# Performance work log

Hardware: AMD Instinct MI355X
Metric: run time of the kernel (lower is better)

The kernel has to match this reference:

```python
import jax, jax.numpy as jnp
import numpy as np

K = 1024
T = 16384
P = 2          # number of lags
N_STAGES = 2   # len(s_list)
EDGE_P = 0.005 # edge density -> avg degree ~5


def setup_inputs() -> dict:
    key = jax.random.key(0)
    kX, kA, ka, kb0, kb1 = jax.random.split(key, 5)
    X = jax.random.normal(kX, (K, T), dtype=jnp.float32)
    # sparse symmetric 0/1 adjacency, zero diagonal
    U = jax.random.uniform(kA, (K, K))
    Ab = (U < EDGE_P)
    Ab = (Ab | Ab.T) & ~jnp.eye(K, dtype=bool)
    A = Ab.astype(jnp.float32)
    alpha = jax.random.normal(ka, (P,), dtype=jnp.float32)
    beta0 = jax.random.normal(kb0, (P,), dtype=jnp.float32)
    beta1 = jax.random.normal(kb1, (P,), dtype=jnp.float32)
    return {"X": X, "A": A, "alpha": alpha, "beta0": beta0, "beta1": beta1}


def _stage_avg_matrices(A):
    """M[r] averages over nodes at shortest-path distance exactly r+1 (rows with
    no stage-r neighbors are all-zero, matching the `if neighbors:` guard)."""
    Ab = A > 0.5
    Af = Ab.astype(jnp.float32)
    reach_prev = jnp.eye(A.shape[0], dtype=bool)  # distance <= 0
    Ms = []
    for _ in range(N_STAGES):
        reach = reach_prev | ((reach_prev.astype(jnp.float32) @ Af) > 0.5)
        exact = reach & ~reach_prev                     # distance == r+1
        exact_f = exact.astype(jnp.float32)
        deg = exact_f.sum(axis=1, keepdims=True)        # (K, 1)
        M = exact_f / jnp.maximum(deg, 1.0)             # zero rows stay zero
        Ms.append(M)
        reach_prev = reach
    return Ms


def reference(X, A, alpha, beta0, beta1):
    K_, T_ = X.shape
    betas = [beta0, beta1]
    Ms = _stage_avg_matrices(A)
    # one dense aggregation per stage over ALL time steps, then slice lags
    MXs = [M @ X for M in Ms]                           # each (K, T)
    Y = jnp.zeros((K_, T_ - P), dtype=X.dtype)
    for lag in range(1, P + 1):
        sl = slice(P - lag, T_ - lag)
        Y = Y + alpha[lag - 1] * X[:, sl]
        for stage in range(N_STAGES):
            Y = Y + betas[stage][lag - 1] * MXs[stage][:, sl]
    return Y
```

## Files before the change

### kernel.cpp

```cpp
#include <hip/hip_runtime.h>

typedef float fx4 __attribute__((ext_vector_type(4)));
typedef short s16x8 __attribute__((ext_vector_type(8)));
typedef __bf16 bfx8 __attribute__((ext_vector_type(8)));

#define KN 1024
#define TT 16384
#define NOUT 16382
#define NKT 32

#define APK_OFF 67108864u
#define B1_OFF  (APK_OFF + 4194304u)

__device__ __forceinline__ unsigned short f2bf(float f) {
  return __builtin_bit_cast(unsigned short, (__bf16)f);
}

__device__ __forceinline__ void gll16(const void* g, void* l) {
  __builtin_amdgcn_global_load_lds(
      (const __attribute__((address_space(1))) void*)g,
      (__attribute__((address_space(3))) void*)l, 16, 0, 0);
}

__global__ __launch_bounds__(256) void k_masks(const float* __restrict__ A,
                                               unsigned* __restrict__ B1) {
  int k = blockIdx.x;
  int tid = threadIdx.x;
  int wv = tid >> 6, lane = tid & 63;
  for (int i = 0; i < 4; ++i) {
    int n = i * 256 + wv * 64 + lane;
    bool bit = (A[(size_t)k * KN + n] > 0.5f) && (n != k);
    unsigned long long m = __ballot(bit);
    if (lane == 0) {
      B1[k * 32 + i * 8 + wv * 2]     = (unsigned)m;
      B1[k * 32 + i * 8 + wv * 2 + 1] = (unsigned)(m >> 32);
    }
  }
}

__global__ __launch_bounds__(256) void k_wp(const unsigned* __restrict__ B1,
                                            const float* __restrict__ alpha,
                                            const float* __restrict__ beta0,
                                            const float* __restrict__ beta1,
                                            const float* __restrict__ X,
                                            unsigned short* __restrict__ Wc,
                                            unsigned short* __restrict__ Bpk) {
  int tid = threadIdx.x;
  if (blockIdx.x >= 1024) {
    int G = (blockIdx.x - 1024) * 256 + tid;
    int col = G & 255;
    int kb  = (G >> 8) & 3;
    int qk  = (G >> 10) & 1;
    int kt  = (G >> 11) & 31;
    int jb  = G >> 16;
    int j   = jb * 256 + col;
    int mbase = kt * 32 + qk * 16 + kb * 4;
    unsigned v[4];
#pragma unroll
    for (int p = 0; p < 4; ++p) {
      int m = mbase + p;
      int j1 = j + 1;
      float f0 = (j1 < TT) ? X[(size_t)m * TT + j1] : 0.0f;
      float f1 = X[(size_t)m * TT + j];
      v[p] = (unsigned)f2bf(f0) | ((unsigned)f2bf(f1) << 16);
    }
    uint4 w; w.x = v[0]; w.y = v[1]; w.z = v[2]; w.w = v[3];
    *reinterpret_cast<uint4*>(Bpk + (size_t)G * 8) = w;
    return;
  }
  __shared__ unsigned reach[32];
  __shared__ unsigned ex2[32];
  __shared__ unsigned short list[1056];
  __shared__ int nl;
  int k = blockIdx.x;
  if (tid == 0) nl = 0;
  if (tid < 32) {
    unsigned r = B1[k * 32 + tid];
    if (tid == (k >> 5)) r |= 1u << (k & 31);
    reach[tid] = r;
    ex2[tid] = 0;
  }
  __syncthreads();
  for (int m = tid; m < KN; m += 256)
    if ((reach[m >> 5] >> (m & 31)) & 1) {
      int i = atomicAdd(&nl, 1);
      list[i] = (unsigned short)m;
    }
  __syncthreads();
  int n2 = nl;
  for (int i = 0; i < n2; ++i) {
    int m = list[i];
    if (tid < 32) ex2[tid] |= B1[m * 32 + tid];
  }
  __syncthreads();
  if (tid < 32) ex2[tid] &= ~reach[tid];
  __syncthreads();
  int d1 = 0, d2 = 0;
  for (int w = 0; w < 32; ++w) { d1 += __popc(reach[w]); d2 += __popc(ex2[w]); }
  d1 -= 1;
  float rd1 = 1.0f / fmaxf((float)d1, 1.0f);
  float rd2 = 1.0f / fmaxf((float)d2, 1.0f);
  float c00 = beta0[0] * rd1, c01 = beta0[1] * rd1;
  float c10 = beta1[0] * rd2, c11 = beta1[1] * rd2;
  float a0 = alpha[0], a1 = alpha[1];
  int mb = k >> 8, rloc = k & 255;
  for (int q = 0; q < 4; ++q) {
    int n = tid * 4 + q;
    bool in1 = (((reach[n >> 5] >> (n & 31)) & 1) != 0) && (n != k);
    bool in2 = ((ex2[n >> 5] >> (n & 31)) & 1) != 0;
    float v0 = (in1 ? c00 : 0.f) + (in2 ? c10 : 0.f) + (n == k ? a0 : 0.f);
    float v1 = (in1 ? c01 : 0.f) + (in2 ? c11 : 0.f) + (n == k ? a1 : 0.f);
    int kt = n >> 5, qk = (n >> 4) & 1, kb = (n >> 2) & 3, ii = (n & 3) * 2;
    size_t idx = ((((size_t)(mb * 32 + kt) * 2 + qk) * 4 + kb) * 256 + rloc) * 8 + ii;
    unsigned pair = (unsigned)f2bf(v0) | ((unsigned)f2bf(v1) << 16);
    *reinterpret_cast<unsigned*>(Wc + idx) = pair;
  }
}

__global__ __launch_bounds__(512, 2) void k_gemm(const char* __restrict__ Apk,
                                                 const char* __restrict__ Bpk,
                                                 float* __restrict__ Y) {
  __shared__ char lds[131072];
  int bid = blockIdx.x;
  int swz = (bid & 7) * 32 + (bid >> 3);
  int jb = swz >> 2, mb = swz & 3;
  int tid = threadIdx.x;
  int lane = tid & 63, wv = tid >> 6;
  int wm = wv >> 2, wn = wv & 3;
  int kb = lane >> 4, ml = lane & 15;
  const char* Asrc = Apk + (size_t)mb * (NKT * 2 * 16384);
  const char* Bsrc = Bpk + (size_t)jb * (NKT * 2 * 16384);

  fx4 acc[2][4][4];
#pragma unroll
  for (int q = 0; q < 2; ++q)
#pragma unroll
    for (int a = 0; a < 4; ++a)
#pragma unroll
      for (int b = 0; b < 4; ++b) acc[q][a][b] = (fx4){0.f, 0.f, 0.f, 0.f};

  auto stage_half = [&](int tile, int isB, int qh) {
    char* dst = lds + (tile & 1) * 65536 + isB * 32768 + qh * 16384;
    const char* src = (isB ? Bsrc : Asrc) + ((size_t)(tile & (NKT - 1)) * 2 + qh) * 16384;
    gll16(src + tid * 16, dst + tid * 16);
    gll16(src + (size_t)(tid + 512) * 16, dst + (tid + 512) * 16);
  };

#define READ_A(dst, t, qk, qm)                                                      \
  do {                                                                              \
    const char* Ah_ = lds + ((t) & 1) * 65536 + (qk) * 16384;                       \
    _Pragma("unroll") for (int mf = 0; mf < 4; ++mf)                                \
      dst[mf] = *(const s16x8*)(Ah_ +                                               \
          (size_t)(kb * 256 + wm * 128 + (qm) * 64 + mf * 16 + ml) * 16);           \
  } while (0)
#define READ_B(dst, t, qk)                                                          \
  do {                                                                              \
    const char* Bh_ = lds + ((t) & 1) * 65536 + 32768 + (qk) * 16384;               \
    _Pragma("unroll") for (int nf = 0; nf < 4; ++nf)                                \
      dst[nf] = *(const s16x8*)(Bh_ +                                               \
          (size_t)(kb * 256 + wn * 64 + nf * 16 + ml) * 16);                        \
  } while (0)
#define MFMA16(acc_, a_, b_)                                                        \
  do {                                                                              \
    _Pragma("unroll") for (int mf = 0; mf < 4; ++mf)                                \
      _Pragma("unroll") for (int nf = 0; nf < 4; ++nf)                              \
        acc_[mf][nf] = __builtin_amdgcn_mfma_f32_16x16x32_bf16(                     \
            __builtin_bit_cast(bfx8, a_[mf]), __builtin_bit_cast(bfx8, b_[nf]),     \
            acc_[mf][nf], 0, 0, 0);                                                 \
  } while (0)

  s16x8 aA[4], aB[4], aC[4], aD[4], bA[4], bB[4];

  stage_half(0, 0, 0); stage_half(0, 1, 0);
  stage_half(0, 0, 1); stage_half(0, 1, 1);
  asm volatile("s_waitcnt vmcnt(0)" ::: "memory");
  __builtin_amdgcn_s_barrier();

  for (int kt = 0; kt < NKT; ++kt) {
    READ_B(bA, kt, 0);
    READ_A(aA, kt, 0, 0);
    stage_half(kt + 1, 0, 0);
    stage_half(kt + 1, 1, 0);
    MFMA16(acc[0], aA, bA);
    READ_A(aB, kt, 0, 1);
    stage_half(kt + 1, 0, 1);
    MFMA16(acc[1], aB, bA);
    READ_B(bB, kt, 1);
    READ_A(aC, kt, 1, 0);
    stage_half(kt + 1, 1, 1);
    MFMA16(acc[0], aC, bB);
    READ_A(aD, kt, 1, 1);
    MFMA16(acc[1], aD, bB);
    asm volatile("s_waitcnt vmcnt(0)" ::: "memory");
    __builtin_amdgcn_s_barrier();
  }

  int c0 = jb * 256 + wn * 64;
  int r0 = mb * 256 + wm * 128;
#pragma unroll
  for (int qm = 0; qm < 2; ++qm)
#pragma unroll
    for (int mf = 0; mf < 4; ++mf)
#pragma unroll
      for (int nf = 0; nf < 4; ++nf) {
        int c = c0 + nf * 16 + ml;
        if (c < NOUT) {
          int r = r0 + qm * 64 + mf * 16 + (lane >> 4) * 4;
#pragma unroll
          for (int i = 0; i < 4; ++i)
            Y[(size_t)(r + i) * NOUT + c] = acc[qm][mf][nf][i];
        }
      }
#undef READ_A
#undef READ_B
#undef MFMA16
}

extern "C" void kernel_launch(void* const* d_in, const int* in_sizes, int n_in,
                              void* d_out, int out_size, void* d_ws, size_t ws_size,
                              hipStream_t stream) {
  const float* X     = (const float*)d_in[0];
  const float* A     = (const float*)d_in[1];
  const float* alpha = (const float*)d_in[2];
  const float* beta0 = (const float*)d_in[3];
  const float* beta1 = (const float*)d_in[4];
  float* Y = (float*)d_out;
  char* ws = (char*)d_ws;
  char* Bpk = ws;
  char* Apk = ws + APK_OFF;
  unsigned* B1 = (unsigned*)(ws + B1_OFF);

  k_masks<<<dim3(1024), dim3(256), 0, stream>>>(A, B1);
  k_wp<<<dim3(17408), dim3(256), 0, stream>>>(B1, alpha, beta0, beta1, X,
                                              (unsigned short*)Apk,
                                              (unsigned short*)Bpk);
  k_gemm<<<dim3(256), dim3(512), 0, stream>>>(Apk, Bpk, Y);
}
```

Baseline: 92.04 us.

## Shrink GEMM tile to 128x128 with 4 waves and half-tile software pipeline

New measurement: 100.5 us. 1.09x slower.

```diff
diff --git a/kernel.cpp b/kernel.cpp
--- a/kernel.cpp
+++ b/kernel.cpp
@@ -48,12 +48,12 @@
   int tid = threadIdx.x;
   if (blockIdx.x >= 1024) {
     int G = (blockIdx.x - 1024) * 256 + tid;
-    int col = G & 255;
-    int kb  = (G >> 8) & 3;
-    int qk  = (G >> 10) & 1;
-    int kt  = (G >> 11) & 31;
-    int jb  = G >> 16;
-    int j   = jb * 256 + col;
+    int col = G & 127;
+    int kb  = (G >> 7) & 3;
+    int qk  = (G >> 9) & 1;
+    int kt  = (G >> 10) & 31;
+    int jb  = G >> 15;
+    int j   = jb * 128 + col;
     int mbase = kt * 32 + qk * 16 + kb * 4;
     unsigned v[4];
 #pragma unroll
@@ -103,7 +103,7 @@
   float c00 = beta0[0] * rd1, c01 = beta0[1] * rd1;
   float c10 = beta1[0] * rd2, c11 = beta1[1] * rd2;
   float a0 = alpha[0], a1 = alpha[1];
-  int mb = k >> 8, rloc = k & 255;
+  int mb = k >> 7, rloc = k & 127;
   for (int q = 0; q < 4; ++q) {
     int n = tid * 4 + q;
     bool in1 = (((reach[n >> 5] >> (n & 31)) & 1) != 0) && (n != k);
@@ -111,106 +111,103 @@
     float v0 = (in1 ? c00 : 0.f) + (in2 ? c10 : 0.f) + (n == k ? a0 : 0.f);
     float v1 = (in1 ? c01 : 0.f) + (in2 ? c11 : 0.f) + (n == k ? a1 : 0.f);
     int kt = n >> 5, qk = (n >> 4) & 1, kb = (n >> 2) & 3, ii = (n & 3) * 2;
-    size_t idx = ((((size_t)(mb * 32 + kt) * 2 + qk) * 4 + kb) * 256 + rloc) * 8 + ii;
+    size_t idx = ((((size_t)(mb * 32 + kt) * 2 + qk) * 4 + kb) * 128 + rloc) * 8 + ii;
     unsigned pair = (unsigned)f2bf(v0) | ((unsigned)f2bf(v1) << 16);
     *reinterpret_cast<unsigned*>(Wc + idx) = pair;
   }
 }
 
-__global__ __launch_bounds__(512, 2) void k_gemm(const char* __restrict__ Apk,
+__global__ __launch_bounds__(256, 2) void k_gemm(const char* __restrict__ Apk,
                                                  const char* __restrict__ Bpk,
                                                  float* __restrict__ Y) {
-  __shared__ char lds[131072];
+  __shared__ char lds[65536];
   int bid = blockIdx.x;
-  int swz = (bid & 7) * 32 + (bid >> 3);
-  int jb = swz >> 2, mb = swz & 3;
+  int swz = (bid & 7) * 128 + (bid >> 3);
+  int jb = swz >> 3, mb = swz & 7;
   int tid = threadIdx.x;
   int lane = tid & 63, wv = tid >> 6;
-  int wm = wv >> 2, wn = wv & 3;
+  int wm = wv >> 1, wn = wv & 1;
   int kb = lane >> 4, ml = lane & 15;
-  const char* Asrc = Apk + (size_t)mb * (NKT * 2 * 16384);
-  const char* Bsrc = Bpk + (size_t)jb * (NKT * 2 * 16384);
-
-  fx4 acc[2][4][4];
-#pragma unroll
-  for (int q = 0; q < 2; ++q)
-#pragma unroll
-    for (int a = 0; a < 4; ++a)
-#pragma unroll
-      for (int b = 0; b < 4; ++b) acc[q][a][b] = (fx4){0.f, 0.f, 0.f, 0.f};
-
-  auto stage_half = [&](int tile, int isB, int qh) {
-    char* dst = lds + (tile & 1) * 65536 + isB * 32768 + qh * 16384;
-    const char* src = (isB ? Bsrc : Asrc) + ((size_t)(tile & (NKT - 1)) * 2 + qh) * 16384;
-    gll16(src + tid * 16, dst + tid * 16);
-    gll16(src + (size_t)(tid + 512) * 16, dst + (tid + 512) * 16);
+  const char* Asrc = Apk + (size_t)mb * (NKT * 2 * 8192);
+  const char* Bsrc = Bpk + (size_t)jb * (NKT * 2 * 8192);
+
+  fx4 acc[4][4];
+#pragma unroll
+  for (int a = 0; a < 4; ++a)
+#pragma unroll
+    for (int b = 0; b < 4; ++b) acc[a][b] = (fx4){0.f, 0.f, 0.f, 0.f};
+
+  auto stage_half = [&](int tile, int h) {
+    char* dst = lds + (tile & 1) * 32768 + h * 8192;
+    const char* srcA = Asrc + ((size_t)(tile & (NKT - 1)) * 2 + h) * 8192;
+    const char* srcB = Bsrc + ((size_t)(tile & (NKT - 1)) * 2 + h) * 8192;
+    gll16(srcA + tid * 16, dst + tid * 16);
+    gll16(srcA + tid * 16 + 4096, dst + tid * 16 + 4096);
+    gll16(srcB + tid * 16, dst + 16384 + tid * 16);
+    gll16(srcB + tid * 16 + 4096, dst + 16384 + tid * 16 + 4096);
   };
 
-#define READ_A(dst, t, qk, qm)                                                      \
+#define READ_A(dst, t, qk)                                                          \
   do {                                                                              \
-    const char* Ah_ = lds + ((t) & 1) * 65536 + (qk) * 16384;                       \
+    const char* Ah_ = lds + ((t) & 1) * 32768 + (qk) * 8192;                        \
     _Pragma("unroll") for (int mf = 0; mf < 4; ++mf)                                \
       dst[mf] = *(const s16x8*)(Ah_ +                                               \
-          (size_t)(kb * 256 + wm * 128 + (qm) * 64 + mf * 16 + ml) * 16);           \
+          (size_t)(kb * 128 + wm * 64 + mf * 16 + ml) * 16);                        \
   } while (0)
 #define READ_B(dst, t, qk)                                                          \
   do {                                                                              \
-    const char* Bh_ = lds + ((t) & 1) * 65536 + 32768 + (qk) * 16384;               \
+    const char* Bh_ = lds + ((t) & 1) * 32768 + 16384 + (qk) * 8192;                \
     _Pragma("unroll") for (int nf = 0; nf < 4; ++nf)                                \
       dst[nf] = *(const s16x8*)(Bh_ +                                               \
-          (size_t)(kb * 256 + wn * 64 + nf * 16 + ml) * 16);                        \
+          (size_t)(kb * 128 + wn * 64 + nf * 16 + ml) * 16);                        \
   } while (0)
-#define MFMA16(acc_, a_, b_)                                                        \
+#define MFMA16(a_, b_)                                                              \
   do {                                                                              \
     _Pragma("unroll") for (int mf = 0; mf < 4; ++mf)                                \
       _Pragma("unroll") for (int nf = 0; nf < 4; ++nf)                              \
-        acc_[mf][nf] = __builtin_amdgcn_mfma_f32_16x16x32_bf16(                     \
+        acc[mf][nf] = __builtin_amdgcn_mfma_f32_16x16x32_bf16(                      \
             __builtin_bit_cast(bfx8, a_[mf]), __builtin_bit_cast(bfx8, b_[nf]),     \
-            acc_[mf][nf], 0, 0, 0);                                                 \
+            acc[mf][nf], 0, 0, 0);                                                  \
   } while (0)
 
-  s16x8 aA[4], aB[4], aC[4], aD[4], bA[4], bB[4];
-
-  stage_half(0, 0, 0); stage_half(0, 1, 0);
-  stage_half(0, 0, 1); stage_half(0, 1, 1);
+  s16x8 aC[4], aN[4], bC[4], bN[4];
+
+  stage_half(0, 0); stage_half(0, 1); stage_half(1, 0);
+  asm volatile("s_waitcnt vmcnt(4)" ::: "memory");
+  __builtin_amdgcn_s_barrier();
+  READ_A(aC, 0, 0);
+  READ_B(bC, 0, 0);
+
+  for (int kt = 0; kt < NKT; ++kt) {
+    READ_A(aN, kt, 1);
+    READ_B(bN, kt, 1);
+    stage_half(kt + 1, 1);
+    MFMA16(aC, bC);
+    asm volatile("s_waitcnt vmcnt(4)" ::: "memory");
+    __builtin_amdgcn_s_barrier();
+    READ_A(aC, kt + 1, 0);
+    READ_B(bC, kt + 1, 0);
+    stage_half(kt + 2, 0);
+    MFMA16(aN, bN);
+    asm volatile("s_waitcnt vmcnt(4)" ::: "memory");
+    __builtin_amdgcn_s_barrier();
+  }
   asm volatile("s_waitcnt vmcnt(0)" ::: "memory");
-  __builtin_amdgcn_s_barrier();
-
-  for (int kt = 0; kt < NKT; ++kt) {
-    READ_B(bA, kt, 0);
-    READ_A(aA, kt, 0, 0);
-    stage_half(kt + 1, 0, 0);
-    stage_half(kt + 1, 1, 0);
-    MFMA16(acc[0], aA, bA);
-    READ_A(aB, kt, 0, 1);
-    stage_half(kt + 1, 0, 1);
-    MFMA16(acc[1], aB, bA);
-    READ_B(bB, kt, 1);
-    READ_A(aC, kt, 1, 0);
-    stage_half(kt + 1, 1, 1);
-    MFMA16(acc[0], aC, bB);
-    READ_A(aD, kt, 1, 1);
-    MFMA16(acc[1], aD, bB);
-    asm volatile("s_waitcnt vmcnt(0)" ::: "memory");
-    __builtin_amdgcn_s_barrier();
-  }
-
-  int c0 = jb * 256 + wn * 64;
-  int r0 = mb * 256 + wm * 128;
-#pragma unroll
-  for (int qm = 0; qm < 2; ++qm)
-#pragma unroll
-    for (int mf = 0; mf < 4; ++mf)
-#pragma unroll
-      for (int nf = 0; nf < 4; ++nf) {
-        int c = c0 + nf * 16 + ml;
-        if (c < NOUT) {
-          int r = r0 + qm * 64 + mf * 16 + (lane >> 4) * 4;
-#pragma unroll
-          for (int i = 0; i < 4; ++i)
-            Y[(size_t)(r + i) * NOUT + c] = acc[qm][mf][nf][i];
-        }
+
+  int c0 = jb * 128 + wn * 64;
+  int r0 = mb * 128 + wm * 64;
+#pragma unroll
+  for (int mf = 0; mf < 4; ++mf)
+#pragma unroll
+    for (int nf = 0; nf < 4; ++nf) {
+      int c = c0 + nf * 16 + ml;
+      if (c < NOUT) {
+        int r = r0 + mf * 16 + (lane >> 4) * 4;
+#pragma unroll
+        for (int i = 0; i < 4; ++i)
+          Y[(size_t)(r + i) * NOUT + c] = acc[mf][nf][i];
       }
+    }
 #undef READ_A
 #undef READ_B
 #undef MFMA16
@@ -234,5 +231,5 @@
   k_wp<<<dim3(17408), dim3(256), 0, stream>>>(B1, alpha, beta0, beta1, X,
                                               (unsigned short*)Apk,
                                               (unsigned short*)Bpk);
-  k_gemm<<<dim3(256), dim3(512), 0, stream>>>(Apk, Bpk, Y);
-}
+  k_gemm<<<dim3(1024), dim3(256), 0, stream>>>(Apk, Bpk, Y);
+}
```

## Pack X once in bf16 and build lag shift inside GEMM from padded LDS tiles

Applied to the files above, without the earlier changes.

After: 92.79 us. About the same (+0.8%).

```diff
diff --git a/kernel.cpp b/kernel.cpp
--- a/kernel.cpp
+++ b/kernel.cpp
@@ -8,8 +8,10 @@
 #define TT 16384
 #define NOUT 16382
 #define NKT 32
-
-#define APK_OFF 67108864u
+#define COLP 16640
+#define HLDS 49664
+
+#define APK_OFF 34078720u
 #define B1_OFF  (APK_OFF + 4194304u)
 
 __device__ __forceinline__ unsigned short f2bf(float f) {
@@ -44,28 +46,25 @@
                                             const float* __restrict__ beta1,
                                             const float* __restrict__ X,
                                             unsigned short* __restrict__ Wc,
-                                            unsigned short* __restrict__ Bpk) {
+                                            unsigned short* __restrict__ Xbf) {
   int tid = threadIdx.x;
   if (blockIdx.x >= 1024) {
-    int G = (blockIdx.x - 1024) * 256 + tid;
-    int col = G & 255;
-    int kb  = (G >> 8) & 3;
-    int qk  = (G >> 10) & 1;
-    int kt  = (G >> 11) & 31;
-    int jb  = G >> 16;
-    int j   = jb * 256 + col;
-    int mbase = kt * 32 + qk * 16 + kb * 4;
+    int p = blockIdx.x - 1024;
+    int o = p & 127;
+    int cb = p >> 7;
+    int c = cb * 256 + tid;
     unsigned v[4];
 #pragma unroll
-    for (int p = 0; p < 4; ++p) {
-      int m = mbase + p;
-      int j1 = j + 1;
-      float f0 = (j1 < TT) ? X[(size_t)m * TT + j1] : 0.0f;
-      float f1 = X[(size_t)m * TT + j];
-      v[p] = (unsigned)f2bf(f0) | ((unsigned)f2bf(f1) << 16);
+    for (int q = 0; q < 4; ++q) {
+      float f0 = 0.f, f1 = 0.f;
+      if (c < TT) {
+        f0 = X[(size_t)(o * 8 + q * 2) * TT + c];
+        f1 = X[(size_t)(o * 8 + q * 2 + 1) * TT + c];
+      }
+      v[q] = (unsigned)f2bf(f0) | ((unsigned)f2bf(f1) << 16);
     }
     uint4 w; w.x = v[0]; w.y = v[1]; w.z = v[2]; w.w = v[3];
-    *reinterpret_cast<uint4*>(Bpk + (size_t)G * 8) = w;
+    *reinterpret_cast<uint4*>(Xbf + ((size_t)o * COLP + c) * 8) = w;
     return;
   }
   __shared__ unsigned reach[32];
@@ -110,17 +109,18 @@
     bool in2 = ((ex2[n >> 5] >> (n & 31)) & 1) != 0;
     float v0 = (in1 ? c00 : 0.f) + (in2 ? c10 : 0.f) + (n == k ? a0 : 0.f);
     float v1 = (in1 ? c01 : 0.f) + (in2 ? c11 : 0.f) + (n == k ? a1 : 0.f);
-    int kt = n >> 5, qk = (n >> 4) & 1, kb = (n >> 2) & 3, ii = (n & 3) * 2;
-    size_t idx = ((((size_t)(mb * 32 + kt) * 2 + qk) * 4 + kb) * 256 + rloc) * 8 + ii;
-    unsigned pair = (unsigned)f2bf(v0) | ((unsigned)f2bf(v1) << 16);
-    *reinterpret_cast<unsigned*>(Wc + idx) = pair;
+    int t = n >> 5, kb2 = (n >> 3) & 3, ii = n & 7;
+    size_t base = (size_t)mb * 524288 +
+                  ((((size_t)t * 2) * 4 + kb2) * 256 + rloc) * 8 + ii;
+    Wc[base] = f2bf(v0);
+    Wc[base + 8192] = f2bf(v1);
   }
 }
 
 __global__ __launch_bounds__(512, 2) void k_gemm(const char* __restrict__ Apk,
-                                                 const char* __restrict__ Bpk,
+                                                 const char* __restrict__ Xbf,
                                                  float* __restrict__ Y) {
-  __shared__ char lds[131072];
+  __shared__ __align__(16) char lds[3 * HLDS];
   int bid = blockIdx.x;
   int swz = (bid & 7) * 32 + (bid >> 3);
   int jb = swz >> 2, mb = swz & 3;
@@ -128,8 +128,7 @@
   int lane = tid & 63, wv = tid >> 6;
   int wm = wv >> 2, wn = wv & 3;
   int kb = lane >> 4, ml = lane & 15;
-  const char* Asrc = Apk + (size_t)mb * (NKT * 2 * 16384);
-  const char* Bsrc = Bpk + (size_t)jb * (NKT * 2 * 16384);
+  const char* Asrc = Apk + (size_t)mb * 1048576;
 
   fx4 acc[2][4][4];
 #pragma unroll
@@ -139,61 +138,85 @@
 #pragma unroll
       for (int b = 0; b < 4; ++b) acc[q][a][b] = (fx4){0.f, 0.f, 0.f, 0.f};
 
-  auto stage_half = [&](int tile, int isB, int qh) {
-    char* dst = lds + (tile & 1) * 65536 + isB * 32768 + qh * 16384;
-    const char* src = (isB ? Bsrc : Asrc) + ((size_t)(tile & (NKT - 1)) * 2 + qh) * 16384;
+  auto stageA = [&](int buf, int ts, int s) {
+    char* dst = lds + buf * HLDS + s * 16384;
+    const char* src = Asrc + ((size_t)ts * 2 + s) * 16384;
     gll16(src + tid * 16, dst + tid * 16);
-    gll16(src + (size_t)(tid + 512) * 16, dst + (tid + 512) * 16);
+    gll16(src + tid * 16 + 8192, dst + tid * 16 + 8192);
   };
-
-#define READ_A(dst, t, qk, qm)                                                      \
+  auto stageB = [&](int buf, int ts) {
+    char* dstB = lds + buf * HLDS + 32768;
+#pragma unroll
+    for (int u2 = 0; u2 < 2; ++u2) {
+      int u = tid + u2 * 512;
+      int kbq = u >> 8, cu = u & 255;
+      const char* src = Xbf + ((size_t)(ts * 4 + kbq) * COLP + jb * 256 + cu) * 16;
+      gll16(src, dstB + (kbq * 264 + cu) * 16);
+    }
+    if ((tid & 127) == 0) {
+      int kbq = tid >> 7;
+      uint4 v = *reinterpret_cast<const uint4*>(
+          Xbf + ((size_t)(ts * 4 + kbq) * COLP + jb * 256 + 256) * 16);
+      *reinterpret_cast<uint4*>(dstB + (kbq * 264 + 256) * 16) = v;
+    }
+  };
+
+#define READ_A(dst, buf, s, qm)                                                     \
   do {                                                                              \
-    const char* Ah_ = lds + ((t) & 1) * 65536 + (qk) * 16384;                       \
+    const char* Ah_ = lds + (buf) * HLDS + (s) * 16384;                             \
     _Pragma("unroll") for (int mf = 0; mf < 4; ++mf)                                \
       dst[mf] = *(const s16x8*)(Ah_ +                                               \
           (size_t)(kb * 256 + wm * 128 + (qm) * 64 + mf * 16 + ml) * 16);           \
   } while (0)
-#define READ_B(dst, t, qk)                                                          \
+#define READ_B(dst, buf, off)                                                       \
   do {                                                                              \
-    const char* Bh_ = lds + ((t) & 1) * 65536 + 32768 + (qk) * 16384;               \
+    const char* Bh_ = lds + (buf) * HLDS + 32768;                                   \
     _Pragma("unroll") for (int nf = 0; nf < 4; ++nf)                                \
       dst[nf] = *(const s16x8*)(Bh_ +                                               \
-          (size_t)(kb * 256 + wn * 64 + nf * 16 + ml) * 16);                        \
+          (size_t)(kb * 264 + wn * 64 + nf * 16 + ml + (off)) * 16);                \
   } while (0)
 #define MFMA16(acc_, a_, b_)                                                        \
   do {                                                                              \
+    __builtin_amdgcn_s_setprio(1);                                                  \
     _Pragma("unroll") for (int mf = 0; mf < 4; ++mf)                                \
       _Pragma("unroll") for (int nf = 0; nf < 4; ++nf)                              \
         acc_[mf][nf] = __builtin_amdgcn_mfma_f32_16x16x32_bf16(                     \
             __builtin_bit_cast(bfx8, a_[mf]), __builtin_bit_cast(bfx8, b_[nf]),     \
             acc_[mf][nf], 0, 0, 0);                                                 \
+    __builtin_amdgcn_s_setprio(0);                                                  \
   } while (0)
 
-  s16x8 aA[4], aB[4], aC[4], aD[4], bA[4], bB[4];
-
-  stage_half(0, 0, 0); stage_half(0, 1, 0);
-  stage_half(0, 0, 1); stage_half(0, 1, 1);
+  s16x8 aA[4], aB[4], bU[4], bV[4];
+
+  stageA(0, 0, 0); stageA(0, 0, 1); stageB(0, 0);
+  stageA(1, 1, 0); stageA(1, 1, 1); stageB(1, 1);
+  asm volatile("s_waitcnt vmcnt(6)" ::: "memory");
+  asm volatile("s_waitcnt lgkmcnt(0)" ::: "memory");
+  __builtin_amdgcn_s_barrier();
+
+  int bR = 0, bW = 2;
+  for (int kt = 0; kt < NKT; ++kt) {
+    int ts2 = (kt + 2) & (NKT - 1);
+    READ_B(bU, bR, 1);
+    READ_A(aA, bR, 0, 0);
+    stageA(bW, ts2, 0);
+    MFMA16(acc[0], aA, bU);
+    READ_A(aB, bR, 0, 1);
+    stageA(bW, ts2, 1);
+    MFMA16(acc[1], aB, bU);
+    READ_B(bV, bR, 0);
+    READ_A(aA, bR, 1, 0);
+    stageB(bW, ts2);
+    MFMA16(acc[0], aA, bV);
+    READ_A(aB, bR, 1, 1);
+    MFMA16(acc[1], aB, bV);
+    asm volatile("s_waitcnt vmcnt(6)" ::: "memory");
+    asm volatile("s_waitcnt lgkmcnt(0)" ::: "memory");
+    __builtin_amdgcn_s_barrier();
+    bR = (bR == 2) ? 0 : bR + 1;
+    bW = (bW == 2) ? 0 : bW + 1;
+  }
   asm volatile("s_waitcnt vmcnt(0)" ::: "memory");
-  __builtin_amdgcn_s_barrier();
-
-  for (int kt = 0; kt < NKT; ++kt) {
-    READ_B(bA, kt, 0);
-    READ_A(aA, kt, 0, 0);
-    stage_half(kt + 1, 0, 0);
-    stage_half(kt + 1, 1, 0);
-    MFMA16(acc[0], aA, bA);
-    READ_A(aB, kt, 0, 1);
-    stage_half(kt + 1, 0, 1);
-    MFMA16(acc[1], aB, bA);
-    READ_B(bB, kt, 1);
-    READ_A(aC, kt, 1, 0);
-    stage_half(kt + 1, 1, 1);
-    MFMA16(acc[0], aC, bB);
-    READ_A(aD, kt, 1, 1);
-    MFMA16(acc[1], aD, bB);
-    asm volatile("s_waitcnt vmcnt(0)" ::: "memory");
-    __builtin_amdgcn_s_barrier();
-  }
 
   int c0 = jb * 256 + wn * 64;
   int r0 = mb * 256 + wm * 128;
@@ -226,13 +249,13 @@
   const float* beta1 = (const float*)d_in[4];
   float* Y = (float*)d_out;
   char* ws = (char*)d_ws;
-  char* Bpk = ws;
+  char* Xbf = ws;
   char* Apk = ws + APK_OFF;
   unsigned* B1 = (unsigned*)(ws + B1_OFF);
 
   k_masks<<<dim3(1024), dim3(256), 0, stream>>>(A, B1);
-  k_wp<<<dim3(17408), dim3(256), 0, stream>>>(B1, alpha, beta0, beta1, X,
-                                              (unsigned short*)Apk,
-                                              (unsigned short*)Bpk);
-  k_gemm<<<dim3(256), dim3(512), 0, stream>>>(Apk, Bpk, Y);
-}
+  k_wp<<<dim3(9344), dim3(256), 0, stream>>>(B1, alpha, beta0, beta1, X,
+                                             (unsigned short*)Apk,
+                                             (unsigned short*)Xbf);
+  k_gemm<<<dim3(256), dim3(512), 0, stream>>>(Apk, Xbf, Y);
+}
```

## Stagger K-half order across wave groups and raise priority around MFMA blocks

Applied to the files above, without the earlier changes.

New measurement: 91.10 us. No clear change (-1.0%).

```diff
diff --git a/kernel.cpp b/kernel.cpp
--- a/kernel.cpp
+++ b/kernel.cpp
@@ -127,6 +127,7 @@
   int tid = threadIdx.x;
   int lane = tid & 63, wv = tid >> 6;
   int wm = wv >> 2, wn = wv & 3;
+  int fl = (wv >> 2) & 1;
   int kb = lane >> 4, ml = lane & 15;
   const char* Asrc = Apk + (size_t)mb * (NKT * 2 * 16384);
   const char* Bsrc = Bpk + (size_t)jb * (NKT * 2 * 16384);
@@ -162,14 +163,27 @@
   } while (0)
 #define MFMA16(acc_, a_, b_)                                                        \
   do {                                                                              \
+    __builtin_amdgcn_s_setprio(1);                                                  \
     _Pragma("unroll") for (int mf = 0; mf < 4; ++mf)                                \
       _Pragma("unroll") for (int nf = 0; nf < 4; ++nf)                              \
         acc_[mf][nf] = __builtin_amdgcn_mfma_f32_16x16x32_bf16(                     \
             __builtin_bit_cast(bfx8, a_[mf]), __builtin_bit_cast(bfx8, b_[nf]),     \
             acc_[mf][nf], 0, 0, 0);                                                 \
-  } while (0)
-
-  s16x8 aA[4], aB[4], aC[4], aD[4], bA[4], bB[4];
+    __builtin_amdgcn_s_setprio(0);                                                  \
+  } while (0)
+
+#define QK_PASS(qk, DO_STAGE)                                                       \
+  do {                                                                              \
+    READ_B(bA, kt, qk);                                                             \
+    READ_A(aA, kt, qk, 0);                                                          \
+    if (DO_STAGE) { stage_half(kt + 1, 0, 0); stage_half(kt + 1, 1, 0); }           \
+    MFMA16(acc[0], aA, bA);                                                         \
+    READ_A(aB, kt, qk, 1);                                                          \
+    if (DO_STAGE) { stage_half(kt + 1, 0, 1); stage_half(kt + 1, 1, 1); }           \
+    MFMA16(acc[1], aB, bA);                                                         \
+  } while (0)
+
+  s16x8 aA[4], aB[4], bA[4];
 
   stage_half(0, 0, 0); stage_half(0, 1, 0);
   stage_half(0, 0, 1); stage_half(0, 1, 1);
@@ -177,20 +191,13 @@
   __builtin_amdgcn_s_barrier();
 
   for (int kt = 0; kt < NKT; ++kt) {
-    READ_B(bA, kt, 0);
-    READ_A(aA, kt, 0, 0);
-    stage_half(kt + 1, 0, 0);
-    stage_half(kt + 1, 1, 0);
-    MFMA16(acc[0], aA, bA);
-    READ_A(aB, kt, 0, 1);
-    stage_half(kt + 1, 0, 1);
-    MFMA16(acc[1], aB, bA);
-    READ_B(bB, kt, 1);
-    READ_A(aC, kt, 1, 0);
-    stage_half(kt + 1, 1, 1);
-    MFMA16(acc[0], aC, bB);
-    READ_A(aD, kt, 1, 1);
-    MFMA16(acc[1], aD, bB);
+    if (fl == 0) {
+      QK_PASS(0, 1);
+      QK_PASS(1, 0);
+    } else {
+      QK_PASS(1, 1);
+      QK_PASS(0, 0);
+    }
     asm volatile("s_waitcnt vmcnt(0)" ::: "memory");
     __builtin_amdgcn_s_barrier();
   }
@@ -214,6 +221,7 @@
 #undef READ_A
 #undef READ_B
 #undef MFMA16
+#undef QK_PASS
 }
 
 extern "C" void kernel_launch(void* const* d_in, const int* in_sizes, int n_in,
```
